# Kernel optimization log

Hardware: AMD Instinct MI355X
Metric: run time of the kernel (lower is better)

Reference implementation:

```python
import jax, jax.numpy as jnp
import numpy as np

Z, N, K, W = 131072, 64, 64, 32


def setup_inputs() -> dict:
    key = jax.random.key(0)
    k1, k2, k3 = jax.random.split(key, 3)
    features = jax.random.normal(k1, (Z, N), dtype=jnp.float32)
    # dense realization of the CG-derived mixing tensor 'wkij'
    mixing_matrix = jax.random.normal(k2, (W, K, N, N), dtype=jnp.float32) * 0.05
    weight = jax.random.normal(k3, (W,), dtype=jnp.float32)
    return {"features": features, "mixing_matrix": mixing_matrix, "weight": weight}


def reference(features, mixing_matrix, weight):
    # torch: einsum('w,wkij,zi,zj->zk', weight, mixing_matrix, features, features)
    # Contract the small path axis w first -> [K, N, N] (cheap, tiny output),
    # then the bilinear square over z. einsum chooses a GEMM-style path; the
    # [Z, N, N] outer-product side is the memory-bound part.
    M = jnp.einsum('w,wkij->kij', weight, mixing_matrix)  # [K, N, N]
    out = jnp.einsum('kij,zi,zj->zk', M, features, features)  # [Z, K]
    return out
```

## Files before the change

### kernel.cpp

```cpp
#include <hip/hip_runtime.h>
#include <stdint.h>

typedef __attribute__((ext_vector_type(8))) short short8;
typedef __attribute__((ext_vector_type(4))) float f32x4;
typedef __attribute__((ext_vector_type(2))) float v2f;

#define NCHUNK 32

__device__ __forceinline__ unsigned short f2bf_rne(float f) {
  unsigned u = __builtin_bit_cast(unsigned, f);
  u += 0x7fffu + ((u >> 16) & 1u);
  return (unsigned short)(u >> 16);
}
__device__ __forceinline__ float bf2f(unsigned short s) {
  return __builtin_bit_cast(float, ((unsigned)s) << 16);
}
__device__ __forceinline__ unsigned pack_bf2(float p0, float p1) {
  return __builtin_amdgcn_perm(__builtin_bit_cast(unsigned, p1),
                               __builtin_bit_cast(unsigned, p0), 0x07060302u);
}
__device__ __forceinline__ void gload16(const void* g, void* l) {
  __builtin_amdgcn_global_load_lds((const __attribute__((address_space(1))) void*)g,
                                   (__attribute__((address_space(3))) void*)l, 16, 0, 0);
}

__global__ __launch_bounds__(256) void prep_kernel(const float* __restrict__ mix,
                                                   const float* __restrict__ wgt,
                                                   unsigned short* __restrict__ Bp) {
  __shared__ float4 red[256];
  const int tid = threadIdx.x;
  const int ws  = tid >> 6;
  const int tt  = tid & 63;
  const int t4  = blockIdx.x * 64 + tt;
  const float4* m4 = (const float4*)mix;
  float ax = 0.f, ay = 0.f, az = 0.f, aw = 0.f;
#pragma unroll
  for (int wi = 0; wi < 8; ++wi) {
    const int w = ws * 8 + wi;
    const float s = wgt[w];
    const float4 v = m4[w * 65536 + t4];
    ax += s * v.x; ay += s * v.y; az += s * v.z; aw += s * v.w;
  }
  red[tid] = (float4){ax, ay, az, aw};
  __syncthreads();
  if (tid < 64) {
    const float4 a = red[tid], b = red[tid + 64], c = red[tid + 128], d = red[tid + 192];
    ushort4 r;
    r.x = f2bf_rne(a.x + b.x + c.x + d.x);
    r.y = f2bf_rne(a.y + b.y + c.y + d.y);
    r.z = f2bf_rne(a.z + b.z + c.z + d.z);
    r.w = f2bf_rne(a.w + b.w + c.w + d.w);
    ((ushort4*)Bp)[blockIdx.x * 64 + tid] = r;
  }
}

__global__ __launch_bounds__(256) void symm_kernel(unsigned short* __restrict__ Bp) {
  unsigned short* B = Bp + (size_t)blockIdx.x * 4096;
  for (int t = threadIdx.x; t < 4096; t += 256) {
    const int i = t >> 6, j = t & 63;
    if (i < j) {
      const int tt = (j << 6) | i;
      const float a = bf2f(B[t]);
      const float b = bf2f(B[tt]);
      B[t]  = f2bf_rne(a + b);
      B[tt] = 0;
    }
  }
}

__global__ __launch_bounds__(256, 3) void gemm_kernel(const float* __restrict__ X,
                                                      const unsigned short* __restrict__ Bp,
                                                      float* __restrict__ out) {
  __shared__ unsigned short ldsB[2][64 * 128];
  __shared__ unsigned short sH[2][2][128];

  const int tid  = threadIdx.x;
  const int lane = tid & 63;
  const int wv   = tid >> 6;
  const int m    = lane & 15;
  const int q    = lane >> 4;
  const int zblk = blockIdx.x * 128;

  auto stageB = [&](int ct, int bf) {
#pragma unroll
    for (int it = 0; it < 4; ++it) {
      const int row = wv * 16 + it * 4 + (lane >> 4);
      const int u   = (lane & 15) ^ (row & 15);
      gload16(Bp + (size_t)row * 4096 + ct * 128 + u * 8,
              &ldsB[bf][(wv * 4 + it) * 512]);
    }
  };

  stageB(0, 0);
  if (tid < 128) {
    const float2 xp = *(const float2*)(X + (size_t)(zblk + tid) * 64);
    const int d  = (tid >> 5) * 16 + (tid & 15);
    const int hf = (tid >> 4) & 1;
    sH[0][0][d * 2 + hf] = f2bf_rne(xp.x);
    sH[0][1][d * 2 + hf] = f2bf_rne(xp.y);
  }

  v2f jv2[2][8];
  {
    const float4* X4g = (const float4*)X;
#pragma unroll
    for (int f = 0; f < 2; ++f) {
      const int zg = zblk + wv * 32 + f * 16 + m;
#pragma unroll
      for (int h = 0; h < 2; ++h) {
        const float4 a = X4g[zg * 16 + h * 8 + q * 2];
        const float4 b = X4g[zg * 16 + h * 8 + q * 2 + 1];
        jv2[f][h * 4 + 0] = v2f{a.x, a.y};
        jv2[f][h * 4 + 1] = v2f{a.z, a.w};
        jv2[f][h * 4 + 2] = v2f{b.x, b.y};
        jv2[f][h * 4 + 3] = v2f{b.z, b.w};
      }
    }
  }

  f32x4 acc[2][4];
#pragma unroll
  for (int f = 0; f < 2; ++f)
#pragma unroll
    for (int g = 0; g < 4; ++g) acc[f][g] = f32x4{0.f, 0.f, 0.f, 0.f};

  __syncthreads();

  auto chunk_body = [&](int c, bool full) {
    const int cn = (c + 1) & (NCHUNK - 1);
    stageB(cn, (c + 1) & 1);
    float2 spre = {0.f, 0.f};
    if (tid < 128)
      spre = *(const float2*)(X + (size_t)(zblk + tid) * 64 + cn * 2);

    const unsigned short* Bl = &ldsB[c & 1][0];
#pragma unroll
    for (int il = 0; il < 2; ++il) {
      const unsigned sv = *(const unsigned*)(&sH[c & 1][il][(wv * 16 + m) * 2]);
      const float s0 = __builtin_bit_cast(float, sv << 16);
      const float s1 = __builtin_bit_cast(float, sv & 0xffff0000u);
      auto hblk = [&](int h) {
        const int u = ((il << 3) + (h << 2) + q) ^ m;
        const unsigned short* bb = Bl + m * 128 + u * 8;
        const short8 b0 = *(const short8*)(bb);
        const short8 b1 = *(const short8*)(bb + 16 * 128);
        const short8 b2 = *(const short8*)(bb + 32 * 128);
        const short8 b3 = *(const short8*)(bb + 48 * 128);
#pragma unroll
        for (int f = 0; f < 2; ++f) {
          const float sf_ = f ? s1 : s0;
          const v2f s2 = v2f{sf_, sf_};
          union { unsigned u[4]; short8 v; } A;
#pragma unroll
          for (int e = 0; e < 4; ++e) {
            const v2f pr = s2 * jv2[f][h * 4 + e];
            A.u[e] = pack_bf2(pr[0], pr[1]);
          }
          acc[f][0] = __builtin_amdgcn_mfma_f32_16x16x32_bf16(A.v, b0, acc[f][0], 0, 0, 0);
          acc[f][1] = __builtin_amdgcn_mfma_f32_16x16x32_bf16(A.v, b1, acc[f][1], 0, 0, 0);
          acc[f][2] = __builtin_amdgcn_mfma_f32_16x16x32_bf16(A.v, b2, acc[f][2], 0, 0, 0);
          acc[f][3] = __builtin_amdgcn_mfma_f32_16x16x32_bf16(A.v, b3, acc[f][3], 0, 0, 0);
        }
      };
      if (full) hblk(0);
      hblk(1);
    }

    if (tid < 128) {
      const int d  = (tid >> 5) * 16 + (tid & 15);
      const int hf = (tid >> 4) & 1;
      sH[(c + 1) & 1][0][d * 2 + hf] = f2bf_rne(spre.x);
      sH[(c + 1) & 1][1][d * 2 + hf] = f2bf_rne(spre.y);
    }
    __syncthreads();
  };

  for (int c = 0; c < 16; ++c)      chunk_body(c, true);
  for (int c = 16; c < NCHUNK; ++c) chunk_body(c, false);

#pragma unroll
  for (int f = 0; f < 2; ++f) {
    const int zr = zblk + wv * 32 + f * 16 + q * 4;
#pragma unroll
    for (int g = 0; g < 4; ++g)
#pragma unroll
      for (int r = 0; r < 4; ++r)
        out[(size_t)(zr + r) * 64 + g * 16 + m] = acc[f][g][r];
  }
}

extern "C" void kernel_launch(void* const* d_in, const int* in_sizes, int n_in,
                              void* d_out, int out_size, void* d_ws, size_t ws_size,
                              hipStream_t stream) {
  const float* X   = (const float*)d_in[0];
  const float* mix = (const float*)d_in[1];
  const float* wgt = (const float*)d_in[2];
  float* out = (float*)d_out;
  unsigned short* Bp = (unsigned short*)d_ws;

  prep_kernel<<<1024, 256, 0, stream>>>(mix, wgt, Bp);
  symm_kernel<<<64, 256, 0, stream>>>(Bp);
  gemm_kernel<<<1024, 256, 0, stream>>>(X, Bp, out);
}
```

Measured before the change: 161.0 us.

## Switch bilinear GEMM to fp16 packed math and split K across wave pairs

Replaces bf16 with fp16 for the precomputed mixing matrix and the outer-product operands. The A-fragment products are now formed with packed half multiplies instead of fp32 multiplies followed by bf16 packing, which removes VALU conversion work from the inner loop. The gemm block grows to 512 threads: each pair of waves shares a z-slice and splits the K output columns, giving more waves to hide latency. Risks are fp16 overflow or precision loss on the products, and a reduced per-wave MFMA count relative to the loads and barriers.

```diff
diff --git a/kernel.cpp b/kernel.cpp
--- a/kernel.cpp
+++ b/kernel.cpp
@@ -1,25 +1,19 @@
 #include <hip/hip_runtime.h>
 #include <stdint.h>
 
-typedef __attribute__((ext_vector_type(8))) short short8;
+typedef __attribute__((ext_vector_type(8))) _Float16 half8;
+typedef __attribute__((ext_vector_type(2))) _Float16 h2;
 typedef __attribute__((ext_vector_type(4))) float f32x4;
-typedef __attribute__((ext_vector_type(2))) float v2f;
 
 #define NCHUNK 32
 
-__device__ __forceinline__ unsigned short f2bf_rne(float f) {
-  unsigned u = __builtin_bit_cast(unsigned, f);
-  u += 0x7fffu + ((u >> 16) & 1u);
-  return (unsigned short)(u >> 16);
+static __device__ __forceinline__ unsigned short f2h(float f) {
+  return __builtin_bit_cast(unsigned short, (_Float16)f);
 }
-__device__ __forceinline__ float bf2f(unsigned short s) {
-  return __builtin_bit_cast(float, ((unsigned)s) << 16);
+static __device__ __forceinline__ float h2f_(unsigned short s) {
+  return (float)__builtin_bit_cast(_Float16, s);
 }
-__device__ __forceinline__ unsigned pack_bf2(float p0, float p1) {
-  return __builtin_amdgcn_perm(__builtin_bit_cast(unsigned, p1),
-                               __builtin_bit_cast(unsigned, p0), 0x07060302u);
-}
-__device__ __forceinline__ void gload16(const void* g, void* l) {
+static __device__ __forceinline__ void gload16(const void* g, void* l) {
   __builtin_amdgcn_global_load_lds((const __attribute__((address_space(1))) void*)g,
                                    (__attribute__((address_space(3))) void*)l, 16, 0, 0);
 }
@@ -46,10 +40,10 @@
   if (tid < 64) {
     const float4 a = red[tid], b = red[tid + 64], c = red[tid + 128], d = red[tid + 192];
     ushort4 r;
-    r.x = f2bf_rne(a.x + b.x + c.x + d.x);
-    r.y = f2bf_rne(a.y + b.y + c.y + d.y);
-    r.z = f2bf_rne(a.z + b.z + c.z + d.z);
-    r.w = f2bf_rne(a.w + b.w + c.w + d.w);
+    r.x = f2h(a.x + b.x + c.x + d.x);
+    r.y = f2h(a.y + b.y + c.y + d.y);
+    r.z = f2h(a.z + b.z + c.z + d.z);
+    r.w = f2h(a.w + b.w + c.w + d.w);
     ((ushort4*)Bp)[blockIdx.x * 64 + tid] = r;
   }
 }
@@ -60,15 +54,15 @@
     const int i = t >> 6, j = t & 63;
     if (i < j) {
       const int tt = (j << 6) | i;
-      const float a = bf2f(B[t]);
-      const float b = bf2f(B[tt]);
-      B[t]  = f2bf_rne(a + b);
+      const float a = h2f_(B[t]);
+      const float b = h2f_(B[tt]);
+      B[t]  = f2h(a + b);
       B[tt] = 0;
     }
   }
 }
 
-__global__ __launch_bounds__(256, 3) void gemm_kernel(const float* __restrict__ X,
+__global__ __launch_bounds__(512, 4) void gemm_kernel(const float* __restrict__ X,
                                                       const unsigned short* __restrict__ Bp,
                                                       float* __restrict__ out) {
   __shared__ unsigned short ldsB[2][64 * 128];
@@ -77,17 +71,20 @@
   const int tid  = threadIdx.x;
   const int lane = tid & 63;
   const int wv   = tid >> 6;
+  const int wz   = wv >> 1;
+  const int wk   = wv & 1;
   const int m    = lane & 15;
   const int q    = lane >> 4;
   const int zblk = blockIdx.x * 128;
 
   auto stageB = [&](int ct, int bf) {
 #pragma unroll
-    for (int it = 0; it < 4; ++it) {
-      const int row = wv * 16 + it * 4 + (lane >> 4);
+    for (int it = 0; it < 2; ++it) {
+      const int seg = wv * 2 + it;
+      const int row = seg * 4 + (lane >> 4);
       const int u   = (lane & 15) ^ (row & 15);
       gload16(Bp + (size_t)row * 4096 + ct * 128 + u * 8,
-              &ldsB[bf][(wv * 4 + it) * 512]);
+              &ldsB[bf][seg * 512]);
     }
   };
 
@@ -96,33 +93,33 @@
     const float2 xp = *(const float2*)(X + (size_t)(zblk + tid) * 64);
     const int d  = (tid >> 5) * 16 + (tid & 15);
     const int hf = (tid >> 4) & 1;
-    sH[0][0][d * 2 + hf] = f2bf_rne(xp.x);
-    sH[0][1][d * 2 + hf] = f2bf_rne(xp.y);
+    sH[0][0][d * 2 + hf] = f2h(xp.x);
+    sH[0][1][d * 2 + hf] = f2h(xp.y);
   }
 
-  v2f jv2[2][8];
+  h2 jh[2][8];
   {
     const float4* X4g = (const float4*)X;
 #pragma unroll
     for (int f = 0; f < 2; ++f) {
-      const int zg = zblk + wv * 32 + f * 16 + m;
+      const int zg = zblk + wz * 32 + f * 16 + m;
 #pragma unroll
       for (int h = 0; h < 2; ++h) {
         const float4 a = X4g[zg * 16 + h * 8 + q * 2];
         const float4 b = X4g[zg * 16 + h * 8 + q * 2 + 1];
-        jv2[f][h * 4 + 0] = v2f{a.x, a.y};
-        jv2[f][h * 4 + 1] = v2f{a.z, a.w};
-        jv2[f][h * 4 + 2] = v2f{b.x, b.y};
-        jv2[f][h * 4 + 3] = v2f{b.z, b.w};
+        jh[f][h * 4 + 0] = h2{(_Float16)a.x, (_Float16)a.y};
+        jh[f][h * 4 + 1] = h2{(_Float16)a.z, (_Float16)a.w};
+        jh[f][h * 4 + 2] = h2{(_Float16)b.x, (_Float16)b.y};
+        jh[f][h * 4 + 3] = h2{(_Float16)b.z, (_Float16)b.w};
       }
     }
   }
 
-  f32x4 acc[2][4];
+  f32x4 acc[2][2];
 #pragma unroll
   for (int f = 0; f < 2; ++f)
 #pragma unroll
-    for (int g = 0; g < 4; ++g) acc[f][g] = f32x4{0.f, 0.f, 0.f, 0.f};
+    for (int g = 0; g < 2; ++g) acc[f][g] = f32x4{0.f, 0.f, 0.f, 0.f};
 
   __syncthreads();
 
@@ -136,30 +133,25 @@
     const unsigned short* Bl = &ldsB[c & 1][0];
 #pragma unroll
     for (int il = 0; il < 2; ++il) {
-      const unsigned sv = *(const unsigned*)(&sH[c & 1][il][(wv * 16 + m) * 2]);
-      const float s0 = __builtin_bit_cast(float, sv << 16);
-      const float s1 = __builtin_bit_cast(float, sv & 0xffff0000u);
+      const unsigned sv = *(const unsigned*)(&sH[c & 1][il][(wz * 16 + m) * 2]);
+      h2 s2f[2];
+      s2f[0] = __builtin_bit_cast(h2, __builtin_amdgcn_perm(sv, sv, 0x01000100u));
+      s2f[1] = __builtin_bit_cast(h2, __builtin_amdgcn_perm(sv, sv, 0x03020302u));
       auto hblk = [&](int h) {
         const int u = ((il << 3) + (h << 2) + q) ^ m;
-        const unsigned short* bb = Bl + m * 128 + u * 8;
-        const short8 b0 = *(const short8*)(bb);
-        const short8 b1 = *(const short8*)(bb + 16 * 128);
-        const short8 b2 = *(const short8*)(bb + 32 * 128);
-        const short8 b3 = *(const short8*)(bb + 48 * 128);
+        const unsigned short* bb = Bl + (wk * 32 + m) * 128 + u * 8;
+        const half8 b0 = *(const half8*)(const void*)(bb);
+        const half8 b1 = *(const half8*)(const void*)(bb + 16 * 128);
 #pragma unroll
         for (int f = 0; f < 2; ++f) {
-          const float sf_ = f ? s1 : s0;
-          const v2f s2 = v2f{sf_, sf_};
-          union { unsigned u[4]; short8 v; } A;
+          union { unsigned u[4]; half8 v; } A;
 #pragma unroll
           for (int e = 0; e < 4; ++e) {
-            const v2f pr = s2 * jv2[f][h * 4 + e];
-            A.u[e] = pack_bf2(pr[0], pr[1]);
+            const h2 pr = s2f[f] * jh[f][h * 4 + e];
+            A.u[e] = __builtin_bit_cast(unsigned, pr);
           }
-          acc[f][0] = __builtin_amdgcn_mfma_f32_16x16x32_bf16(A.v, b0, acc[f][0], 0, 0, 0);
-          acc[f][1] = __builtin_amdgcn_mfma_f32_16x16x32_bf16(A.v, b1, acc[f][1], 0, 0, 0);
-          acc[f][2] = __builtin_amdgcn_mfma_f32_16x16x32_bf16(A.v, b2, acc[f][2], 0, 0, 0);
-          acc[f][3] = __builtin_amdgcn_mfma_f32_16x16x32_bf16(A.v, b3, acc[f][3], 0, 0, 0);
+          acc[f][0] = __builtin_amdgcn_mfma_f32_16x16x32_f16(A.v, b0, acc[f][0], 0, 0, 0);
+          acc[f][1] = __builtin_amdgcn_mfma_f32_16x16x32_f16(A.v, b1, acc[f][1], 0, 0, 0);
         }
       };
       if (full) hblk(0);
@@ -169,8 +161,8 @@
     if (tid < 128) {
       const int d  = (tid >> 5) * 16 + (tid & 15);
       const int hf = (tid >> 4) & 1;
-      sH[(c + 1) & 1][0][d * 2 + hf] = f2bf_rne(spre.x);
-      sH[(c + 1) & 1][1][d * 2 + hf] = f2bf_rne(spre.y);
+      sH[(c + 1) & 1][0][d * 2 + hf] = f2h(spre.x);
+      sH[(c + 1) & 1][1][d * 2 + hf] = f2h(spre.y);
     }
     __syncthreads();
   };
@@ -180,12 +172,12 @@
 
 #pragma unroll
   for (int f = 0; f < 2; ++f) {
-    const int zr = zblk + wv * 32 + f * 16 + q * 4;
+    const int zr = zblk + wz * 32 + f * 16 + q * 4;
 #pragma unroll
-    for (int g = 0; g < 4; ++g)
+    for (int g = 0; g < 2; ++g)
 #pragma unroll
       for (int r = 0; r < 4; ++r)
-        out[(size_t)(zr + r) * 64 + g * 16 + m] = acc[f][g][r];
+        out[(size_t)(zr + r) * 64 + wk * 32 + g * 16 + m] = acc[f][g][r];
   }
 }
 
@@ -200,5 +192,5 @@
 
   prep_kernel<<<1024, 256, 0, stream>>>(mix, wgt, Bp);
   symm_kernel<<<64, 256, 0, stream>>>(Bp);
-  gemm_kernel<<<1024, 256, 0, stream>>>(X, Bp, out);
+  gemm_kernel<<<1024, 512, 0, stream>>>(X, Bp, out);
 }
```

Result: slower. 164.8 us (+2.4%).
